# Optimization experiments

Measured on AMD Instinct MI355X. Metric: run time of the kernel, lower is better.

Reference implementation:

```python
import jax
import jax.numpy as jnp
import numpy as np

IN_FEATS = 784
HIDDEN_DIM = 1024
BATCH = 1024


def setup_inputs() -> dict:
    key = jax.random.key(0)
    k_px, k_W, k_c, k_V, k_b = jax.random.split(key, 5)
    pixels = jax.random.uniform(k_px, (BATCH, IN_FEATS), dtype=jnp.float32)
    W = jax.random.normal(k_W, (HIDDEN_DIM, IN_FEATS), dtype=jnp.float32)
    c = jax.random.normal(k_c, (HIDDEN_DIM,), dtype=jnp.float32)
    V = jax.random.normal(k_V, (IN_FEATS, HIDDEN_DIM), dtype=jnp.float32)
    b = jax.random.normal(k_b, (IN_FEATS,), dtype=jnp.float32)
    return {"pixels": pixels, "W": W, "c": c, "V": V, "b": b}


def reference(pixels, W, c, V, b):
    # pixels: [B, D]; W: [H, D]; c: [H]; V: [D, H]; b: [D]
    B = pixels.shape[0]
    a0 = jnp.broadcast_to(c[None, :], (B, c.shape[0]))  # [B, H]

    def step(a, inp):
        w_col, v_row, b_i, x_i = inp  # [H], [H], [], [B]
        h = jax.nn.sigmoid(a)                     # [B, H]
        pred_i = b_i + h @ v_row                  # [B]
        a_next = a + w_col[None, :] * x_i[:, None]  # rank-1 accumulator update
        return a_next, pred_i

    xs = (W.T, V, b, pixels.T)  # each leading dim D (scan over visible units)
    _, preds = jax.lax.scan(step, a0, xs)  # preds: [D, B]
    return preds.T  # [B, D]
```

## Files before the change

kernel.cpp:

```cpp
#include <hip/hip_runtime.h>
#include <stdint.h>

#define B_ 1024
#define D_ 784
#define H_ 1024
#define BH_ (B_ * H_)
#define LOG2E 1.4426950408889634f


__device__ __forceinline__ unsigned short bf16_rne(float x) {
    unsigned b = __float_as_uint(x);
    return (unsigned short)((b + 0x7FFFu + ((b >> 16) & 1u)) >> 16);
}

__device__ __forceinline__ int seg_bound(int s) {
    const int b[7] = {0, 136, 272, 400, 528, 656, 784};
    return b[s];
}

__global__ __launch_bounds__(256) void prep(const float* __restrict__ V,
                                            const float* __restrict__ W,
                                            const float* __restrict__ px,
                                            unsigned short* __restrict__ VWb,
                                            float* __restrict__ G) {
    __shared__ float smem[1056];
    const int t = threadIdx.x;

    if (blockIdx.x < 800) {
        int i0 = (blockIdx.x % 25) * 32;
        int h0 = (blockIdx.x / 25) * 32;
        int tx = t & 31, ty = t >> 5;
        int hb = h0 >> 8, hr = h0 & 255;
#pragma unroll
        for (int j = 0; j < 4; ++j) {
            int i = i0 + ty + j * 8;
            if (i < D_)
                VWb[((size_t)i * 4 + hb) * 512 + hr + tx] = bf16_rne(V[(size_t)i * H_ + h0 + tx]);
        }
#pragma unroll
        for (int j = 0; j < 4; ++j) {
            int h = h0 + ty + j * 8;
            int i = i0 + tx;
            float v = 0.f;
            if (i < D_) v = W[(size_t)h * D_ + i] * LOG2E;
            smem[(ty + j * 8) * 33 + tx] = v;
        }
        __syncthreads();
#pragma unroll
        for (int j = 0; j < 4; ++j) {
            int i = i0 + ty + j * 8;
            if (i < D_)
                VWb[((size_t)i * 4 + hb) * 512 + 256 + hr + tx] = bf16_rne(smem[tx * 33 + ty + j * 8]);
        }
    } else {
        float* xs = smem;
        float* ws = smem + 512;
        int idx = blockIdx.x - 800;
        int r   = idx >> 8;
        int b0  = (idx & 15) * 64;
        int h0  = ((idx >> 4) & 15) * 64;
        int j0s = seg_bound(r), j1s = seg_bound(r + 1);

        const int tb = t >> 4, th = t & 15;
        float acc[4][4];
#pragma unroll
        for (int bi = 0; bi < 4; ++bi)
#pragma unroll
            for (int hh = 0; hh < 4; ++hh) acc[bi][hh] = 0.f;

        const int xb = t >> 3;
        const int xj = t & 7;
        const int wh = t >> 1, wj = (t & 1) * 4;

        for (int j0 = j0s; j0 < j1s; j0 += 8) {
            float xv0 = px[(size_t)(b0 + xb) * D_ + j0 + xj];
            float xv1 = px[(size_t)(b0 + 32 + xb) * D_ + j0 + xj];
            float4 wv = make_float4(0, 0, 0, 0);
            if (t < 128) wv = *(const float4*)(W + (size_t)(h0 + wh) * D_ + j0 + wj);
            __syncthreads();
            xs[xj * 64 + xb]      = xv0;
            xs[xj * 64 + 32 + xb] = xv1;
            if (t < 128) {
                ws[(wj + 0) * 64 + wh] = wv.x * LOG2E;
                ws[(wj + 1) * 64 + wh] = wv.y * LOG2E;
                ws[(wj + 2) * 64 + wh] = wv.z * LOG2E;
                ws[(wj + 3) * 64 + wh] = wv.w * LOG2E;
            }
            __syncthreads();
#pragma unroll
            for (int jj = 0; jj < 8; ++jj) {
                float4 xq = *(float4*)&xs[jj * 64 + tb * 4];
                float4 wq = *(float4*)&ws[jj * 64 + th * 4];
                float xa[4] = {xq.x, xq.y, xq.z, xq.w};
                float wa[4] = {wq.x, wq.y, wq.z, wq.w};
#pragma unroll
                for (int bi = 0; bi < 4; ++bi)
#pragma unroll
                    for (int hh = 0; hh < 4; ++hh)
                        acc[bi][hh] = fmaf(xa[bi], wa[hh], acc[bi][hh]);
            }
        }
        float* dst = G + (size_t)r * BH_;
#pragma unroll
        for (int bi = 0; bi < 4; ++bi) {
            float4 o = make_float4(acc[bi][0], acc[bi][1], acc[bi][2], acc[bi][3]);
            *(float4*)(dst + (size_t)(b0 + tb * 4 + bi) * H_ + h0 + th * 4) = o;
        }
    }
}

template <int CTRL>
__device__ __forceinline__ float dpp_add(float p) {
    int s = __builtin_amdgcn_update_dpp(0, __float_as_int(p), CTRL, 0xf, 0xf, true);
    return p + __int_as_float(s);
}
__device__ __forceinline__ float reduce_halves(float p) {
    p = dpp_add<0x111>(p);
    p = dpp_add<0x112>(p);
    p = dpp_add<0x114>(p);
    p = dpp_add<0x118>(p);
    p = dpp_add<0x142>(p);
    return p;
}

__device__ __forceinline__ void cvt8(uint4 u, float4& a, float4& b) {
    a.x = __uint_as_float(u.x << 16);
    a.y = __uint_as_float(u.x);
    a.z = __uint_as_float(u.y << 16);
    a.w = __uint_as_float(u.y);
    b.x = __uint_as_float(u.z << 16);
    b.y = __uint_as_float(u.z);
    b.z = __uint_as_float(u.w << 16);
    b.w = __uint_as_float(u.w);
}

__global__ __launch_bounds__(256, 8) void nade_main(
    const float* __restrict__ px,
    const float* __restrict__ c,
    const unsigned short* __restrict__ VWb,
    const float* __restrict__ G,
    const float* __restrict__ bias,
    float* __restrict__ out)
{
    __shared__ float4 red[2][4][2];

    const int lane = threadIdx.x & 63;
    const int wid  = threadIdx.x >> 6;
    const int bid  = blockIdx.x;
    const int s    = bid % 6;
    const int rp   = bid / 6;
    const int half = lane >> 5;
    const int row  = rp * 2 + half;
    const int hl   = lane & 31;
    const int h0   = wid * 256 + hl * 8;

    const int i0s = seg_bound(s), i1s = seg_bound(s + 1);

    float A[8];
    {
        float4 c0 = *(const float4*)(c + h0);
        float4 c1 = *(const float4*)(c + h0 + 4);
        A[0] = c0.x * LOG2E; A[1] = c0.y * LOG2E; A[2] = c0.z * LOG2E; A[3] = c0.w * LOG2E;
        A[4] = c1.x * LOG2E; A[5] = c1.y * LOG2E; A[6] = c1.z * LOG2E; A[7] = c1.w * LOG2E;
        for (int r = 0; r < s; ++r) {
            const float* gp = G + (size_t)r * BH_ + (size_t)row * H_ + h0;
            float4 g0 = *(const float4*)(gp);
            float4 g1 = *(const float4*)(gp + 4);
            A[0] += g0.x; A[1] += g0.y; A[2] += g0.z; A[3] += g0.w;
            A[4] += g1.x; A[5] += g1.y; A[6] += g1.z; A[7] += g1.w;
        }
    }

    const float* xp = px + (size_t)row * D_;
    const uint4* vw = (const uint4*)VWb + ((size_t)i0s * 4 + wid) * 64 + hl;

    auto step8 = [&A](const float4& v0, const float4& v1,
                      const float4& w0, const float4& w1, float xi) -> float {
        float va[8] = {v0.x, v0.y, v0.z, v0.w, v1.x, v1.y, v1.z, v1.w};
        float wa[8] = {w0.x, w0.y, w0.z, w0.w, w1.x, w1.y, w1.z, w1.w};
        float q[8];
#pragma unroll
        for (int k = 0; k < 8; ++k) {
            float e = __builtin_amdgcn_exp2f(fminf(15.f, -A[k]));
            q[k] = 1.f + e;
            A[k] = fmaf(wa[k], xi, A[k]);
        }
        float a01 = fmaf(va[0], q[1], va[1] * q[0]);
        float a23 = fmaf(va[2], q[3], va[3] * q[2]);
        float a45 = fmaf(va[4], q[5], va[5] * q[4]);
        float a67 = fmaf(va[6], q[7], va[7] * q[6]);
        float q01 = q[0] * q[1], q23 = q[2] * q[3];
        float q45 = q[4] * q[5], q67 = q[6] * q[7];
        float n0123 = fmaf(a01, q23, a23 * q01);
        float n4567 = fmaf(a45, q67, a67 * q45);
        float q0123 = q01 * q23, q4567 = q45 * q67;
        float r = __builtin_amdgcn_rcpf(q0123 * q4567);
        float n = fmaf(n0123, q4567, n4567 * q0123);
        return n * r;
    };

    uint4 uv = vw[0], uw = vw[32];
    vw += 256;
    float4 xq = *(const float4*)(xp + i0s);

    for (int ib = i0s; ib < i1s; ib += 4) {
        int xb = (ib + 4 < i1s) ? (ib + 4) : i0s;
        float4 xq_n = *(const float4*)(xp + xb);
        float xa[4] = {xq.x, xq.y, xq.z, xq.w};
        float pr[4];
#pragma unroll
        for (int j = 0; j < 4; ++j) {
            uint4 uvn = vw[0], uwn = vw[32];
            vw += 256;
            float4 v0, v1, w0, w1;
            cvt8(uv, v0, v1);
            cvt8(uw, w0, w1);
            float p = step8(v0, v1, w0, w1, xa[j]);
            pr[j] = reduce_halves(p);
            uv = uvn; uw = uwn;
        }
        const int par = (ib >> 2) & 1;
        if (hl == 31) red[par][wid][half] = make_float4(pr[0], pr[1], pr[2], pr[3]);
        __syncthreads();
        if (threadIdx.x < 2) {
            float4 b4 = *(const float4*)(bias + ib);
            float4 p0 = red[par][0][threadIdx.x];
            float4 p1 = red[par][1][threadIdx.x];
            float4 p2 = red[par][2][threadIdx.x];
            float4 p3 = red[par][3][threadIdx.x];
            float4 o;
            o.x = b4.x + ((p0.x + p1.x) + (p2.x + p3.x));
            o.y = b4.y + ((p0.y + p1.y) + (p2.y + p3.y));
            o.z = b4.z + ((p0.z + p1.z) + (p2.z + p3.z));
            o.w = b4.w + ((p0.w + p1.w) + (p2.w + p3.w));
            *(float4*)(out + (size_t)(rp * 2 + threadIdx.x) * D_ + ib) = o;
        }
        xq = xq_n;
    }
}

extern "C" void kernel_launch(void* const* d_in, const int* in_sizes, int n_in,
                              void* d_out, int out_size, void* d_ws, size_t ws_size,
                              hipStream_t stream) {
    const float* px   = (const float*)d_in[0];
    const float* W    = (const float*)d_in[1];
    const float* c    = (const float*)d_in[2];
    const float* V    = (const float*)d_in[3];
    const float* bias = (const float*)d_in[4];
    float* out = (float*)d_out;

    unsigned short* VWb = (unsigned short*)d_ws;
    float* G    = (float*)((char*)d_ws + (size_t)788 * 4096);

    prep<<<dim3(2080), 256, 0, stream>>>(V, W, px, VWb, G);

    nade_main<<<dim3(3072), 256, 0, stream>>>(px, c, VWb, G, bias, out);
}
```

Before: 324.0 us.

## Use four D-segments, 8-step inner batches, and segment-major block order

Cuts the scan split over D from six segments to four, so there are fewer prefix-sum G blocks in prep and fewer blocks in the main kernel. The main loop now handles 8 visible units per barrier instead of 4, which halves the __syncthreads and reduction rounds. Blocks are now ordered segment-major, so concurrent blocks share the same VW segment. The trade-off is a longer serial chain per block and less parallelism (2048 blocks instead of 3072), plus higher register pressure from the larger unroll.

New measurement: 729.3 us. +125.1%, slower.

```diff
diff --git a/kernel.cpp b/kernel.cpp
--- a/kernel.cpp
+++ b/kernel.cpp
@@ -14,7 +14,7 @@
 }
 
 __device__ __forceinline__ int seg_bound(int s) {
-    const int b[7] = {0, 136, 272, 400, 528, 656, 784};
+    const int b[5] = {0, 200, 392, 592, 784};
     return b[s];
 }
 
@@ -142,13 +142,13 @@
     const float* __restrict__ bias,
     float* __restrict__ out)
 {
-    __shared__ float4 red[2][4][2];
+    __shared__ float4 red[2][4][2][2];
 
     const int lane = threadIdx.x & 63;
     const int wid  = threadIdx.x >> 6;
     const int bid  = blockIdx.x;
-    const int s    = bid % 6;
-    const int rp   = bid / 6;
+    const int s    = bid >> 9;
+    const int rp   = bid & 511;
     const int half = lane >> 5;
     const int row  = rp * 2 + half;
     const int hl   = lane & 31;
@@ -201,15 +201,17 @@
 
     uint4 uv = vw[0], uw = vw[32];
     vw += 256;
-    float4 xq = *(const float4*)(xp + i0s);
-
-    for (int ib = i0s; ib < i1s; ib += 4) {
-        int xb = (ib + 4 < i1s) ? (ib + 4) : i0s;
-        float4 xq_n = *(const float4*)(xp + xb);
-        float xa[4] = {xq.x, xq.y, xq.z, xq.w};
-        float pr[4];
-#pragma unroll
-        for (int j = 0; j < 4; ++j) {
+    float4 xqA = *(const float4*)(xp + i0s);
+    float4 xqB = *(const float4*)(xp + i0s + 4);
+
+    for (int ib = i0s; ib < i1s; ib += 8) {
+        int xb = (ib + 8 < i1s) ? (ib + 8) : i0s;
+        float4 xqA_n = *(const float4*)(xp + xb);
+        float4 xqB_n = *(const float4*)(xp + xb + 4);
+        float xa[8] = {xqA.x, xqA.y, xqA.z, xqA.w, xqB.x, xqB.y, xqB.z, xqB.w};
+        float pr[8];
+#pragma unroll
+        for (int j = 0; j < 8; ++j) {
             uint4 uvn = vw[0], uwn = vw[32];
             vw += 256;
             float4 v0, v1, w0, w1;
@@ -219,23 +221,28 @@
             pr[j] = reduce_halves(p);
             uv = uvn; uw = uwn;
         }
-        const int par = (ib >> 2) & 1;
-        if (hl == 31) red[par][wid][half] = make_float4(pr[0], pr[1], pr[2], pr[3]);
+        const int par = (ib >> 3) & 1;
+        if (hl == 31) {
+            red[par][wid][half][0] = make_float4(pr[0], pr[1], pr[2], pr[3]);
+            red[par][wid][half][1] = make_float4(pr[4], pr[5], pr[6], pr[7]);
+        }
         __syncthreads();
-        if (threadIdx.x < 2) {
-            float4 b4 = *(const float4*)(bias + ib);
-            float4 p0 = red[par][0][threadIdx.x];
-            float4 p1 = red[par][1][threadIdx.x];
-            float4 p2 = red[par][2][threadIdx.x];
-            float4 p3 = red[par][3][threadIdx.x];
+        if (threadIdx.x < 4) {
+            const int g  = threadIdx.x >> 1;
+            const int hf = threadIdx.x & 1;
+            float4 b4 = *(const float4*)(bias + ib + g * 4);
+            float4 p0 = red[par][0][hf][g];
+            float4 p1 = red[par][1][hf][g];
+            float4 p2 = red[par][2][hf][g];
+            float4 p3 = red[par][3][hf][g];
             float4 o;
             o.x = b4.x + ((p0.x + p1.x) + (p2.x + p3.x));
             o.y = b4.y + ((p0.y + p1.y) + (p2.y + p3.y));
             o.z = b4.z + ((p0.z + p1.z) + (p2.z + p3.z));
             o.w = b4.w + ((p0.w + p1.w) + (p2.w + p3.w));
-            *(float4*)(out + (size_t)(rp * 2 + threadIdx.x) * D_ + ib) = o;
-        }
-        xq = xq_n;
+            *(float4*)(out + (size_t)(rp * 2 + hf) * D_ + ib + g * 4) = o;
+        }
+        xqA = xqA_n; xqB = xqB_n;
     }
 }
 
@@ -252,7 +259,7 @@
     unsigned short* VWb = (unsigned short*)d_ws;
     float* G    = (float*)((char*)d_ws + (size_t)788 * 4096);
 
-    prep<<<dim3(2080), 256, 0, stream>>>(V, W, px, VWb, G);
-
-    nade_main<<<dim3(3072), 256, 0, stream>>>(px, c, VWb, G, bias, out);
-}
+    prep<<<dim3(1568), 256, 0, stream>>>(V, W, px, VWb, G);
+
+    nade_main<<<dim3(2048), 256, 0, stream>>>(px, c, VWb, G, bias, out);
+}
```
